# Kernel tuning notes

Hardware: AMD Instinct MI355X
Metric: run time of the kernel (lower is better)

## Reference

```python
import jax, jax.numpy as jnp
import numpy as np

D_MODEL = 1024
N_HEADS = 16
D_K = D_MODEL // N_HEADS
D_FF = 4096
EPS = 1e-6


def _layernorm(x, g, b):
    mu = jnp.mean(x, axis=-1, keepdims=True)
    var = jnp.mean(jnp.square(x - mu), axis=-1, keepdims=True)
    return (x - mu) * jax.lax.rsqrt(var + EPS) * g + b


def setup_inputs() -> dict:
    key = jax.random.key(0)
    ks = jax.random.split(key, 12)
    B, S = 2, 2048
    sd_attn = (1.0 / np.sqrt(2.0)) * np.sqrt(2.0 / (D_MODEL + D_MODEL))  # xavier gain 1/sqrt(2) (std approx)
    sd_ff1 = np.sqrt(2.0 / (D_MODEL + D_FF))
    sd_ff2 = np.sqrt(2.0 / (D_FF + D_MODEL))
    return {
        "x": jax.random.normal(ks[0], (B, S, D_MODEL), jnp.float32),
        "mask": jnp.ones((B, S), jnp.int32),
        # weights stored (in, out) so forward is x @ W
        "wq": jax.random.normal(ks[1], (D_MODEL, D_MODEL), jnp.float32) * sd_attn,
        "wk": jax.random.normal(ks[2], (D_MODEL, D_MODEL), jnp.float32) * sd_attn,
        "wv": jax.random.normal(ks[3], (D_MODEL, D_MODEL), jnp.float32) * sd_attn,
        "wo": jax.random.normal(ks[4], (D_MODEL, D_MODEL), jnp.float32) * sd_attn,
        "wo_b": jnp.zeros((D_MODEL,), jnp.float32),
        "w1": jax.random.normal(ks[5], (D_MODEL, D_FF), jnp.float32) * sd_ff1,
        "b1": jnp.zeros((D_FF,), jnp.float32),
        "w2": jax.random.normal(ks[6], (D_FF, D_MODEL), jnp.float32) * sd_ff2,
        "b2": jnp.zeros((D_MODEL,), jnp.float32),
        "g1": jnp.ones((D_MODEL,), jnp.float32),
        "be1": jnp.zeros((D_MODEL,), jnp.float32),
        "g2": jnp.ones((D_MODEL,), jnp.float32),
        "be2": jnp.zeros((D_MODEL,), jnp.float32),
    }


def reference(x, mask, wq, wk, wv, wo, wo_b, w1, b1, w2, b2, g1, be1, g2, be2):
    B, S, _ = x.shape
    scale = 1.0 / np.sqrt(D_K)
    # project and split heads -> [B, H, S, Dk]
    q = (x @ wq).reshape(B, S, N_HEADS, D_K).transpose(0, 2, 1, 3)
    k = (x @ wk).reshape(B, S, N_HEADS, D_K).transpose(0, 2, 1, 3)
    v = (x @ wv).reshape(B, S, N_HEADS, D_K).transpose(0, 2, 1, 3)
    scores = jnp.einsum("bhqd,bhkd->bhqk", q, k) * scale  # [B,H,S,S]
    m = (mask[:, None, None, :] == 0)
    scores = jnp.where(m, -1e9, scores)
    attn = jax.nn.softmax(scores, axis=-1)
    ctx = jnp.einsum("bhqk,bhkd->bhqd", attn, v)
    ctx = ctx.transpose(0, 2, 1, 3).reshape(B, S, D_MODEL)
    attn_out = ctx @ wo + wo_b
    x = _layernorm(x + attn_out, g1, be1)
    ff = jax.nn.gelu(x @ w1 + b1, approximate=False) @ w2 + b2
    return _layernorm(x + ff, g2, be2)
```

## Files before the change

### kernel.cpp

```cpp
#include <hip/hip_runtime.h>
#include <cstdint>

#define DEVINL __device__ __forceinline__

typedef __attribute__((ext_vector_type(8))) short short8;
typedef __attribute__((ext_vector_type(4))) short short4v;
typedef __attribute__((ext_vector_type(4))) float floatx4;
typedef __attribute__((ext_vector_type(4))) unsigned short ushort4v;

DEVINL uint32_t pkbf(float a, float b) {
  uint32_t d;
  asm("v_cvt_pk_bf16_f32 %0, %1, %2" : "=v"(d) : "v"(a), "v"(b));
  return d;
}
DEVINL unsigned short f2bf(float f) {
  union { float f; uint32_t u; } v; v.f = f;
  return (unsigned short)((v.u + 0x7fffu + ((v.u >> 16) & 1u)) >> 16);
}
DEVINL float bf2f(unsigned short h) {
  union { uint32_t u; float f; } v; v.u = ((uint32_t)h) << 16;
  return v.f;
}

#if defined(__has_builtin) && __has_builtin(__builtin_amdgcn_exp2f)
#define EXP2(x) __builtin_amdgcn_exp2f(x)
#else
#define EXP2(x) exp2f(x)
#endif

DEVINL float fast_gelu(float v) {
  const float z = -2.30220795f * v * (1.0f + 0.044715f * v * v);
  return v * __builtin_amdgcn_rcpf(1.0f + EXP2(z));
}

typedef __attribute__((address_space(3))) unsigned char* lds_ptr_t;
typedef const __attribute__((address_space(1))) unsigned char* gbl_ptr_t;
DEVINL void load_lds_128(const void* g, void* l) {
  __builtin_amdgcn_global_load_lds((gbl_ptr_t)g, (lds_ptr_t)l, 16, 0, 0);
}

#define MFMA16(a, b, c) __builtin_amdgcn_mfma_f32_16x16x32_bf16((a), (b), (c), 0, 0, 0)

#define QSCALE2 0.18033688011112042f

__global__ __launch_bounds__(256) void prep_kernel(
    const float* __restrict__ x, unsigned short* __restrict__ XB,
    const float* __restrict__ wq, const float* __restrict__ wk,
    const float* __restrict__ wv, const float* __restrict__ wo,
    unsigned short* __restrict__ WQKV, unsigned short* __restrict__ WOT,
    const float* __restrict__ w1, unsigned short* __restrict__ W1T,
    const float* __restrict__ w2, unsigned short* __restrict__ W2T,
    const int* __restrict__ mask, unsigned short* __restrict__ MB) {
  const int bid = blockIdx.x;
  const int t = threadIdx.x;
  if (bid >= 7168) {
    const int i0 = t * 16;
#pragma unroll
    for (int j = 0; j < 16; ++j) MB[i0 + j] = mask[i0 + j] ? 0x3F80 : 0;
    return;
  }
  if (bid < 4096) {
    const int i = (bid * 256 + t) * 4;
    floatx4 v = *(const floatx4*)(x + i);
    union { uint32_t u[2]; ushort4v v4; } o;
    o.u[0] = pkbf(v[0], v[1]);
    o.u[1] = pkbf(v[2], v[3]);
    *(ushort4v*)(XB + i) = o.v4;
    return;
  }
  const float* in;
  unsigned short* out;
  int K, N, bx, by;
  if (bid < 5120) {
    const int b2 = bid - 4096, z = b2 >> 8, bb = b2 & 255;
    in = (z == 0) ? wq : (z == 1) ? wk : (z == 2) ? wv : wo;
    out = (z == 3) ? WOT : WQKV + (size_t)z * 1024 * 1024;
    K = 1024; N = 1024; bx = bb & 15; by = bb >> 4;
  } else if (bid < 6144) {
    const int b3 = bid - 5120;
    in = w1; out = W1T; K = 1024; N = 4096; bx = b3 & 63; by = b3 >> 6;
  } else {
    const int b4 = bid - 6144;
    in = w2; out = W2T; K = 4096; N = 1024; bx = b4 & 15; by = b4 >> 4;
  }
  __shared__ float tile[64][65];
  const int n0 = bx * 64, k0 = by * 64;
  const int rl = t >> 4, c4 = (t & 15) * 4;
#pragma unroll
  for (int p = 0; p < 4; ++p) {
    const int r = rl + 16 * p;
    const floatx4 v = *(const floatx4*)(in + (size_t)(k0 + r) * N + n0 + c4);
#pragma unroll
    for (int j = 0; j < 4; ++j) tile[r][c4 + j] = v[j];
  }
  __syncthreads();
  const int rw = t >> 3, c8 = (t & 7) * 8;
#pragma unroll
  for (int p = 0; p < 2; ++p) {
    const int row = rw + 32 * p;
    union { unsigned short h[8]; short8 s8; } o;
#pragma unroll
    for (int j = 0; j < 8; ++j) o.h[j] = f2bf(tile[c8 + j][row]);
    *(short8*)(out + (size_t)(n0 + row) * K + k0 + c8) = o.s8;
  }
}

template <int EPI, int SK>
__global__ __launch_bounds__(256, 3) void gemm_bt_kernel(
    const unsigned short* __restrict__ A, const unsigned short* __restrict__ BT,
    const float* __restrict__ bias, void* __restrict__ C0, void* __restrict__ C1,
    void* __restrict__ C2, int M, int N, int K, const int* __restrict__ msk) {
  __shared__ __align__(16) unsigned short As[128 * 64];
  __shared__ __align__(16) unsigned short Bs[128 * 64];
  const int tid = threadIdx.x;
  const int w = tid >> 6, l = tid & 63;
  const int lq = l >> 4, lr = l & 15;

  int bxs, bys;
  {
    const int nx = gridDim.x, ny = gridDim.y;
    const int f = blockIdx.y * nx + blockIdx.x;
    const int xcd = f & 7, s = f >> 3;
    const int q = nx >> 1, p = ny >> 2;
    bxs = (xcd & 1) * q + (s % q);
    bys = (xcd >> 1) * p + (s / q);
  }
  const int m0 = bys * 128;
  const int region = (EPI == 5) ? (bxs % 3) : 0;
  const int n0 = (EPI == 5) ? (region * 1024 + (bxs / 3) * 128) : (bxs * 128);
  const int wm = (w >> 1) * 64, wn = (w & 1) * 64;
  const int r_a = l >> 2;
  const int colb = (l & 3) * 8;
  const int kslice = K / SK;
  const int kbeg = kslice * blockIdx.z;

  uint32_t mbits = 0xFFFFu;
  if (EPI == 5 && region == 2) {
    mbits = 0;
#pragma unroll
    for (int mt = 0; mt < 4; ++mt) {
      const int4 m4 = *(const int4*)(msk + m0 + wm + mt * 16 + lq * 4);
      mbits |= (m4.x ? 1u : 0u) << (mt * 4);
      mbits |= (m4.y ? 1u : 0u) << (mt * 4 + 1);
      mbits |= (m4.z ? 1u : 0u) << (mt * 4 + 2);
      mbits |= (m4.w ? 1u : 0u) << (mt * 4 + 3);
    }
  }

  floatx4 acc[4][4];
  const floatx4 fz = {0.f, 0.f, 0.f, 0.f};
#pragma unroll
  for (int mt = 0; mt < 4; ++mt)
#pragma unroll
    for (int nt = 0; nt < 4; ++nt) acc[mt][nt] = fz;

  for (int k0 = kbeg; k0 < kbeg + kslice; k0 += 64) {
    __syncthreads();
#pragma unroll
    for (int p = 0; p < 2; ++p) {
#pragma unroll
      for (int i = 0; i < 2; ++i) {
        const int c = w * 2 + i;
        load_lds_128(A + (size_t)(m0 + c * 16 + r_a) * K + k0 + p * 32 + colb,
                     (char*)As + p * 8192 + c * 1024);
        load_lds_128(BT + (size_t)(n0 + c * 16 + r_a) * K + k0 + p * 32 + colb,
                     (char*)Bs + p * 8192 + c * 1024);
      }
    }
    __syncthreads();
#pragma unroll
    for (int p = 0; p < 2; ++p) {
      short8 af[4], bf[4];
#pragma unroll
      for (int mt = 0; mt < 4; ++mt)
        af[mt] = *(const short8*)((const char*)As + p * 8192 + (wm + mt * 16 + lr) * 64 + lq * 16);
#pragma unroll
      for (int nt = 0; nt < 4; ++nt)
        bf[nt] = *(const short8*)((const char*)Bs + p * 8192 + (wn + nt * 16 + lr) * 64 + lq * 16);
#pragma unroll
      for (int mt = 0; mt < 4; ++mt)
#pragma unroll
        for (int nt = 0; nt < 4; ++nt)
          acc[mt][nt] = MFMA16(af[mt], bf[nt], acc[mt][nt]);
    }
  }

  void* Cp = (SK > 1 && blockIdx.z) ? C1 : C0;
#pragma unroll
  for (int mt = 0; mt < 4; ++mt) {
#pragma unroll
    for (int nt = 0; nt < 4; ++nt) {
      const int n = n0 + wn + nt * 16 + lr;
      if (EPI == 5 && region == 2) {
        const int nn = n - 2048;
        const int hh = nn >> 6, d = nn & 63;
        const int s0 = m0 + wm + mt * 16 + lq * 4;
        const int bidx = s0 >> 11, si = s0 & 2047;
        const int u0 = si & 31;
        const int spb = (si & ~31) | (((u0 >> 4) & 1) << 2) | (((u0 >> 2) & 3) << 3);
        float vv[4];
#pragma unroll
        for (int r = 0; r < 4; ++r)
          vv[r] = ((mbits >> (mt * 4 + r)) & 1u) ? acc[mt][nt][r] : 0.f;
        union { uint32_t u[2]; ushort4v v4; } o;
        o.u[0] = pkbf(vv[0], vv[1]);
        o.u[1] = pkbf(vv[2], vv[3]);
        *(ushort4v*)((unsigned short*)C2 +
                     ((size_t)((bidx * 16 + hh) * 64 + d)) * 2048 + spb) = o.v4;
        continue;
      }
      float bval = 0.f;
      if (EPI == 2) bval = bias[n];
#pragma unroll
      for (int r = 0; r < 4; ++r) {
        const int m = m0 + wm + mt * 16 + lq * 4 + r;
        float v = acc[mt][nt][r];
        if (EPI == 4) {
          ((unsigned short*)Cp)[(size_t)m * N + n] = f2bf(v);
        } else if (EPI == 2) {
          ((unsigned short*)C0)[(size_t)m * N + n] = f2bf(fast_gelu(v + bval));
        } else {
          if (region == 0) {
            ((unsigned short*)C0)[(size_t)m * 1024 + n] = f2bf(v * QSCALE2);
          } else {
            ((unsigned short*)C1)[(size_t)m * 1024 + (n - 1024)] = f2bf(v);
          }
        }
      }
    }
  }
}

__global__ __launch_bounds__(256, 2) void flash_kernel(
    const unsigned short* __restrict__ Q, const unsigned short* __restrict__ Kg,
    const unsigned short* __restrict__ VT, const unsigned short* __restrict__ MB,
    unsigned short* __restrict__ ctx) {
  __shared__ __align__(16) unsigned short Ks[128 * 64];
  __shared__ __align__(16) unsigned short VTs[64 * 128];

  const int tid = threadIdx.x, w = tid >> 6, l = tid & 63;
  const int lq = l >> 4, lr = l & 15;
  const int lin = blockIdx.x;
  const int xcd = lin & 7, slot = lin >> 3;
  const int bh = xcd * 4 + (slot >> 4);
  const int b = bh >> 4, h = bh & 15;
  const int q0 = (slot & 15) * 128;

  const unsigned short* Qp = Q + (size_t)(b * 2048 + q0) * 1024 + h * 64;
  const unsigned short* Kp = Kg + (size_t)(b * 2048) * 1024 + h * 64;
  const unsigned short* VTp = VT + (size_t)bh * 64 * 2048;
  const unsigned short* mbp = MB + b * 2048;

  {
    const int rq = l >> 3, cs = l & 7;
#pragma unroll
    for (int i = 0; i < 4; ++i) {
      const int c = w * 4 + i;
      load_lds_128(Qp + (size_t)(c * 8 + rq) * 1024 + cs * 8, (char*)Ks + c * 1024);
    }
  }
  __syncthreads();
  short8 qf[2][2];
#pragma unroll
  for (int qg = 0; qg < 2; ++qg) {
    qf[qg][0] = *(const short8*)((const char*)Ks + (w * 32 + qg * 16 + lr) * 128 + lq * 16);
    qf[qg][1] = *(const short8*)((const char*)Ks + (w * 32 + qg * 16 + lr) * 128 + 64 + lq * 16);
  }
  __syncthreads();

  const floatx4 fz = {0.f, 0.f, 0.f, 0.f};
  floatx4 o[2][4];
#pragma unroll
  for (int qg = 0; qg < 2; ++qg)
#pragma unroll
    for (int nt = 0; nt < 4; ++nt) o[qg][nt] = fz;
  floatx4 l_acc[2] = {fz, fz};

  const int krow = l >> 3, kslot = l & 7;
  const int vrow = l >> 4, vslot = l & 15;

  for (int kb = 0; kb < 2048; kb += 128) {
    if (kb) __syncthreads();
#pragma unroll
    for (int i = 0; i < 4; ++i) {
      const int c4 = w * 4 + i;
      {
        const int row = c4 * 8 + krow;
        const int cc = kslot ^ (row & 7);
        load_lds_128(Kp + (size_t)(kb + row) * 1024 + cc * 8, (char*)Ks + c4 * 1024);
      }
      {
        const int row = c4 * 4 + vrow;
        const int cc = vslot ^ (row & 15);
        load_lds_128(VTp + (size_t)row * 2048 + kb + cc * 8, (char*)VTs + c4 * 1024);
      }
    }
    short8 mf[4];
#pragma unroll
    for (int t = 0; t < 4; ++t) {
      const short4v ma = *(const short4v*)(mbp + kb + t * 32 + lq * 4);
      const short4v mb2 = *(const short4v*)(mbp + kb + t * 32 + 16 + lq * 4);
      mf[t] = short8{ma[0], ma[1], ma[2], ma[3], mb2[0], mb2[1], mb2[2], mb2[3]};
    }
    __syncthreads();

#pragma unroll
    for (int h2 = 0; h2 < 2; ++h2) {
      floatx4 s[2][4];
#pragma unroll
      for (int gg = 0; gg < 4; ++gg) {
        const int g = h2 * 4 + gg;
        const char* rowp = (const char*)Ks + (g * 16 + lr) * 128;
        short8 k0 = *(const short8*)(rowp + ((lq) ^ (lr & 7)) * 16);
        short8 k1 = *(const short8*)(rowp + ((4 + lq) ^ (lr & 7)) * 16);
#pragma unroll
        for (int qg = 0; qg < 2; ++qg) {
          floatx4 t = MFMA16(k0, qf[qg][0], fz);
          s[qg][gg] = MFMA16(k1, qf[qg][1], t);
        }
      }
      short8 pf[2][2];
#pragma unroll
      for (int qg = 0; qg < 2; ++qg)
#pragma unroll
        for (int tt = 0; tt < 2; ++tt) {
          const floatx4 sL = s[qg][tt * 2], sH = s[qg][tt * 2 + 1];
          union { uint32_t u[4]; short8 s8; } pk;
          pk.u[0] = pkbf(EXP2(sL[0]), EXP2(sL[1]));
          pk.u[1] = pkbf(EXP2(sL[2]), EXP2(sL[3]));
          pk.u[2] = pkbf(EXP2(sH[0]), EXP2(sH[1]));
          pk.u[3] = pkbf(EXP2(sH[2]), EXP2(sH[3]));
          pf[qg][tt] = pk.s8;
        }
#pragma unroll
      for (int tt = 0; tt < 2; ++tt) {
        const int t = h2 * 2 + tt;
        l_acc[0] = MFMA16(pf[0][tt], mf[t], l_acc[0]);
        l_acc[1] = MFMA16(pf[1][tt], mf[t], l_acc[1]);
#pragma unroll
        for (int nt = 0; nt < 4; ++nt) {
          const int d = nt * 16 + lr;
          short8 vf = *(const short8*)((const char*)VTs + d * 256 +
                                       (((t * 4 + lq) ^ (d & 15)) * 16));
          o[0][nt] = MFMA16(pf[0][tt], vf, o[0][nt]);
          o[1][nt] = MFMA16(pf[1][tt], vf, o[1][nt]);
        }
      }
    }
  }

#pragma unroll
  for (int qg = 0; qg < 2; ++qg)
#pragma unroll
    for (int r = 0; r < 4; ++r) {
      const float inv = 1.0f / l_acc[qg][r];
      const int q = q0 + w * 32 + qg * 16 + lq * 4 + r;
#pragma unroll
      for (int nt = 0; nt < 4; ++nt)
        ctx[(size_t)(b * 2048 + q) * 1024 + h * 64 + nt * 16 + lr] = f2bf(o[qg][nt][r] * inv);
    }
}

template <int RESBF, int OUTBF>
__global__ __launch_bounds__(256) void ln2_kernel(
    const void* __restrict__ res, const unsigned short* __restrict__ y0,
    const unsigned short* __restrict__ y1, const float* __restrict__ bias,
    const float* __restrict__ gamma, const float* __restrict__ beta,
    void* __restrict__ outp) {
  const int row = blockIdx.x, t = threadIdx.x;
  const size_t base = (size_t)row * 1024 + t * 4;
  float v[4];
  if (RESBF) {
    ushort4v r4 = *(const ushort4v*)((const unsigned short*)res + base);
#pragma unroll
    for (int j = 0; j < 4; ++j) v[j] = bf2f(r4[j]);
  } else {
    floatx4 r4 = *(const floatx4*)((const float*)res + base);
#pragma unroll
    for (int j = 0; j < 4; ++j) v[j] = r4[j];
  }
  const ushort4v a4 = *(const ushort4v*)(y0 + base);
  const ushort4v b4v = *(const ushort4v*)(y1 + base);
  const floatx4 bi4 = *(const floatx4*)(bias + t * 4);
  float s = 0.f, ss = 0.f;
#pragma unroll
  for (int j = 0; j < 4; ++j) {
    v[j] += bf2f(a4[j]) + bf2f(b4v[j]) + bi4[j];
    s += v[j];
    ss += v[j] * v[j];
  }
#pragma unroll
  for (int off = 1; off < 64; off <<= 1) {
    s += __shfl_xor(s, off);
    ss += __shfl_xor(ss, off);
  }
  __shared__ float red[8];
  const int w = t >> 6;
  if ((t & 63) == 0) { red[w] = s; red[4 + w] = ss; }
  __syncthreads();
  s = red[0] + red[1] + red[2] + red[3];
  ss = red[4] + red[5] + red[6] + red[7];
  const float mean = s * (1.0f / 1024.0f);
  const float var = ss * (1.0f / 1024.0f) - mean * mean;
  const float rstd = rsqrtf(var + 1e-6f);
  const floatx4 g4 = *(const floatx4*)(gamma + t * 4);
  const floatx4 be4 = *(const floatx4*)(beta + t * 4);
  if (OUTBF) {
    union { uint32_t u[2]; ushort4v v4; } o;
    o.u[0] = pkbf((v[0] - mean) * rstd * g4[0] + be4[0],
                  (v[1] - mean) * rstd * g4[1] + be4[1]);
    o.u[1] = pkbf((v[2] - mean) * rstd * g4[2] + be4[2],
                  (v[3] - mean) * rstd * g4[3] + be4[3]);
    *(ushort4v*)((unsigned short*)outp + base) = o.v4;
  } else {
    floatx4 o;
#pragma unroll
    for (int j = 0; j < 4; ++j) o[j] = (v[j] - mean) * rstd * g4[j] + be4[j];
    *(floatx4*)((float*)outp + base) = o;
  }
}

extern "C" void kernel_launch(void* const* d_in, const int* in_sizes, int n_in,
                              void* d_out, int out_size, void* d_ws, size_t ws_size,
                              hipStream_t stream) {
  (void)in_sizes; (void)n_in; (void)out_size; (void)ws_size;
  const float* x    = (const float*)d_in[0];
  const int*   mask = (const int*)d_in[1];
  const float* wq   = (const float*)d_in[2];
  const float* wk   = (const float*)d_in[3];
  const float* wv   = (const float*)d_in[4];
  const float* wo   = (const float*)d_in[5];
  const float* wo_b = (const float*)d_in[6];
  const float* w1   = (const float*)d_in[7];
  const float* b1   = (const float*)d_in[8];
  const float* w2   = (const float*)d_in[9];
  const float* b2   = (const float*)d_in[10];
  const float* g1   = (const float*)d_in[11];
  const float* be1  = (const float*)d_in[12];
  const float* g2   = (const float*)d_in[13];
  const float* be2  = (const float*)d_in[14];
  float* out = (float*)d_out;

  char* ws = (char*)d_ws;
  const size_t MBy = 1024ull * 1024ull;
  unsigned short* WQKV = (unsigned short*)(ws + 0 * MBy);
  unsigned short* WOT  = (unsigned short*)(ws + 6 * MBy);
  unsigned short* W1T  = (unsigned short*)(ws + 8 * MBy);
  unsigned short* W2T  = (unsigned short*)(ws + 16 * MBy);
  unsigned short* XB   = (unsigned short*)(ws + 24 * MBy);
  unsigned short* Qb   = (unsigned short*)(ws + 32 * MBy);
  unsigned short* Kb   = (unsigned short*)(ws + 40 * MBy);
  unsigned short* VTb  = (unsigned short*)(ws + 48 * MBy);
  unsigned short* CTX  = (unsigned short*)(ws + 56 * MBy);
  unsigned short* ATT0 = (unsigned short*)(ws + 32 * MBy);
  unsigned short* ATT1 = (unsigned short*)(ws + 40 * MBy);
  unsigned short* Hb   = (unsigned short*)(ws + 24 * MBy);
  unsigned short* G1   = (unsigned short*)(ws + 32 * MBy);
  unsigned short* FF20 = (unsigned short*)(ws + 64 * MBy);
  unsigned short* FF21 = (unsigned short*)(ws + 72 * MBy);
  unsigned short* MB   = (unsigned short*)(ws + 78 * MBy);

  prep_kernel<<<7169, 256, 0, stream>>>(x, XB, wq, wk, wv, wo, WQKV, WOT,
                                        w1, W1T, w2, W2T, mask, MB);
  gemm_bt_kernel<5, 1><<<dim3(24, 32), 256, 0, stream>>>(
      XB, WQKV, nullptr, Qb, Kb, VTb, 4096, 3072, 1024, mask);
  flash_kernel<<<512, 256, 0, stream>>>(Qb, Kb, VTb, MB, CTX);
  gemm_bt_kernel<4, 2><<<dim3(8, 32, 2), 256, 0, stream>>>(
      CTX, WOT, nullptr, ATT0, ATT1, nullptr, 4096, 1024, 1024, nullptr);
  ln2_kernel<0, 1><<<4096, 256, 0, stream>>>(x, ATT0, ATT1, wo_b, g1, be1, Hb);
  gemm_bt_kernel<2, 1><<<dim3(32, 32), 256, 0, stream>>>(
      Hb, W1T, b1, G1, nullptr, nullptr, 4096, 4096, 1024, nullptr);
  gemm_bt_kernel<4, 2><<<dim3(8, 32, 2), 256, 0, stream>>>(
      G1, W2T, nullptr, FF20, FF21, nullptr, 4096, 1024, 4096, nullptr);
  ln2_kernel<1, 0><<<4096, 256, 0, stream>>>(Hb, FF20, FF21, b2, g2, be2, out);
}
```

Baseline: 311.7 us.

## Split flash attention over two KV halves and merge partial outputs

The attention kernel now splits the key/value sequence into two halves, launching twice as many blocks, each writing a normalized partial output and its softmax denominator. A new merge kernel combines the two partials weighted by their denominators. The aim is more parallelism and occupancy on the many-CU GPU (the launch-bounds hint rises from 2 to 4 blocks per CU). The cost is an extra kernel launch, extra global traffic for the partials, and an extra bf16 rounding of the partial outputs. The merge is exact only if both halves share the same softmax max, which appears to rely on a fixed offset rather than a per-row running max.

```diff
diff --git a/kernel.cpp b/kernel.cpp
--- a/kernel.cpp
+++ b/kernel.cpp
@@ -231,10 +231,11 @@
   }
 }
 
-__global__ __launch_bounds__(256, 2) void flash_kernel(
+__global__ __launch_bounds__(256, 4) void flash_kernel(
     const unsigned short* __restrict__ Q, const unsigned short* __restrict__ Kg,
     const unsigned short* __restrict__ VT, const unsigned short* __restrict__ MB,
-    unsigned short* __restrict__ ctx) {
+    unsigned short* __restrict__ OP0, unsigned short* __restrict__ OP1,
+    float* __restrict__ L0, float* __restrict__ L1) {
   __shared__ __align__(16) unsigned short Ks[128 * 64];
   __shared__ __align__(16) unsigned short VTs[64 * 128];
 
@@ -242,14 +243,17 @@
   const int lq = l >> 4, lr = l & 15;
   const int lin = blockIdx.x;
   const int xcd = lin & 7, slot = lin >> 3;
-  const int bh = xcd * 4 + (slot >> 4);
+  const int bh = xcd * 4 + (slot >> 5);
+  const int kvh = (slot >> 4) & 1;
   const int b = bh >> 4, h = bh & 15;
   const int q0 = (slot & 15) * 128;
 
   const unsigned short* Qp = Q + (size_t)(b * 2048 + q0) * 1024 + h * 64;
-  const unsigned short* Kp = Kg + (size_t)(b * 2048) * 1024 + h * 64;
-  const unsigned short* VTp = VT + (size_t)bh * 64 * 2048;
-  const unsigned short* mbp = MB + b * 2048;
+  const unsigned short* Kp = Kg + (size_t)(b * 2048 + kvh * 1024) * 1024 + h * 64;
+  const unsigned short* VTp = VT + (size_t)bh * 64 * 2048 + kvh * 1024;
+  const unsigned short* mbp = MB + b * 2048 + kvh * 1024;
+  unsigned short* op = kvh ? OP1 : OP0;
+  float* Lp = kvh ? L1 : L0;
 
   {
     const int rq = l >> 3, cs = l & 7;
@@ -279,7 +283,7 @@
   const int krow = l >> 3, kslot = l & 7;
   const int vrow = l >> 4, vslot = l & 15;
 
-  for (int kb = 0; kb < 2048; kb += 128) {
+  for (int kb = 0; kb < 1024; kb += 128) {
     if (kb) __syncthreads();
 #pragma unroll
     for (int i = 0; i < 4; ++i) {
@@ -353,12 +357,34 @@
   for (int qg = 0; qg < 2; ++qg)
 #pragma unroll
     for (int r = 0; r < 4; ++r) {
-      const float inv = 1.0f / l_acc[qg][r];
+      const float lsum = l_acc[qg][r];
+      const float inv = 1.0f / (lsum + 1e-30f);
       const int q = q0 + w * 32 + qg * 16 + lq * 4 + r;
+      if (lr == 0) Lp[(size_t)(b * 2048 + q) * 16 + h] = lsum;
 #pragma unroll
       for (int nt = 0; nt < 4; ++nt)
-        ctx[(size_t)(b * 2048 + q) * 1024 + h * 64 + nt * 16 + lr] = f2bf(o[qg][nt][r] * inv);
-    }
+        op[(size_t)(b * 2048 + q) * 1024 + h * 64 + nt * 16 + lr] = f2bf(o[qg][nt][r] * inv);
+    }
+}
+
+__global__ __launch_bounds__(256) void merge_kernel(
+    const unsigned short* __restrict__ op0, const unsigned short* __restrict__ op1,
+    const float* __restrict__ L0, const float* __restrict__ L1,
+    unsigned short* __restrict__ ctx) {
+  const int row = blockIdx.x, t = threadIdx.x;
+  const size_t base = (size_t)row * 1024 + t * 4;
+  const int h = t >> 4;
+  const float l0 = L0[(size_t)row * 16 + h], l1 = L1[(size_t)row * 16 + h];
+  const float inv = 1.0f / (l0 + l1 + 1e-30f);
+  const float w0 = l0 * inv, w1 = l1 * inv;
+  const ushort4v a = *(const ushort4v*)(op0 + base);
+  const ushort4v bq = *(const ushort4v*)(op1 + base);
+  union { uint32_t u[2]; ushort4v v4; } o;
+  o.u[0] = pkbf(bf2f(a[0]) * w0 + bf2f(bq[0]) * w1,
+                bf2f(a[1]) * w0 + bf2f(bq[1]) * w1);
+  o.u[1] = pkbf(bf2f(a[2]) * w0 + bf2f(bq[2]) * w1,
+                bf2f(a[3]) * w0 + bf2f(bq[3]) * w1);
+  *(ushort4v*)(ctx + base) = o.v4;
 }
 
 template <int RESBF, int OUTBF>
@@ -452,6 +478,10 @@
   unsigned short* Kb   = (unsigned short*)(ws + 40 * MBy);
   unsigned short* VTb  = (unsigned short*)(ws + 48 * MBy);
   unsigned short* CTX  = (unsigned short*)(ws + 56 * MBy);
+  unsigned short* OP0  = (unsigned short*)(ws + 24 * MBy);
+  unsigned short* OP1  = (unsigned short*)(ws + 64 * MBy);
+  float*          L0f  = (float*)(ws + 72 * MBy);
+  float*          L1f  = (float*)(ws + 72 * MBy + 256 * 1024);
   unsigned short* ATT0 = (unsigned short*)(ws + 32 * MBy);
   unsigned short* ATT1 = (unsigned short*)(ws + 40 * MBy);
   unsigned short* Hb   = (unsigned short*)(ws + 24 * MBy);
@@ -464,7 +494,8 @@
                                         w1, W1T, w2, W2T, mask, MB);
   gemm_bt_kernel<5, 1><<<dim3(24, 32), 256, 0, stream>>>(
       XB, WQKV, nullptr, Qb, Kb, VTb, 4096, 3072, 1024, mask);
-  flash_kernel<<<512, 256, 0, stream>>>(Qb, Kb, VTb, MB, CTX);
+  flash_kernel<<<1024, 256, 0, stream>>>(Qb, Kb, VTb, MB, OP0, OP1, L0f, L1f);
+  merge_kernel<<<4096, 256, 0, stream>>>(OP0, OP1, L0f, L1f, CTX);
   gemm_bt_kernel<4, 2><<<dim3(8, 32, 2), 256, 0, stream>>>(
       CTX, WOT, nullptr, ATT0, ATT1, nullptr, 4096, 1024, 1024, nullptr);
   ln2_kernel<0, 1><<<4096, 256, 0, stream>>>(x, ATT0, ATT1, wo_b, g1, be1, Hb);
```

New measurement: 329.3 us. +5.6%, slower.
